# Kernel tuning notes

Hardware: AMD Instinct MI355X
Metric: run time of the kernel (lower is better)

Reference implementation:

```python
import jax, jax.numpy as jnp
import numpy as np

H = 8          # number of heads
D_MODEL = 512  # model dim
D_HEAD = D_MODEL // H


def setup_inputs() -> dict:
    key = jax.random.key(0)
    ks = jax.random.split(key, 8)
    B, C, L = 4, D_MODEL, 2048
    s = 1.0 / np.sqrt(D_MODEL)
    return {
        "x1": jax.random.normal(ks[0], (B, C, L), dtype=jnp.float32),
        "x2": jax.random.normal(ks[1], (B, C, L), dtype=jnp.float32),
        "Wq": jax.random.uniform(ks[2], (D_MODEL, D_MODEL), jnp.float32, -s, s),
        "bq": jax.random.uniform(ks[3], (D_MODEL,), jnp.float32, -s, s),
        "Wk": jax.random.uniform(ks[4], (D_MODEL, D_MODEL), jnp.float32, -s, s),
        "bk": jax.random.uniform(ks[5], (D_MODEL,), jnp.float32, -s, s),
        "Wv": jax.random.uniform(ks[6], (D_MODEL, D_MODEL), jnp.float32, -s, s),
        "bv": jax.random.uniform(ks[7], (D_MODEL,), jnp.float32, -s, s),
    }


def reference(x1, x2, Wq, bq, Wk, bk, Wv, bv):
    # x1, x2: [B, C, L] with C == d_model (3D branch of the torch module)
    B, C, L = x1.shape
    x1t = jnp.swapaxes(x1, 1, 2)  # [B, L, C]
    x2t = jnp.swapaxes(x2, 1, 2)  # [B, L, C]

    def proj(x, W, b):  # torch Linear: x @ W.T + b, then split heads
        y = jnp.einsum('blc,dc->bld', x, W) + b          # [B, L, C]
        return y.reshape(B, -1, H, D_HEAD).transpose(0, 2, 1, 3)  # [B, H, L, d]

    q = proj(x1t, Wq, bq)
    k = proj(x2t, Wk, bk)
    v = proj(x2t, Wv, bv)

    scores = jnp.einsum('bhqd,bhkd->bhqk', q, k) / jnp.sqrt(
        jnp.asarray(D_HEAD, dtype=q.dtype))
    attn = jax.nn.softmax(scores, axis=-1)
    out = jnp.einsum('bhqk,bhkd->bhqd', attn, v)          # [B, H, L, d]

    # transpose(1,2).view(B,-1,C).transpose(1,2) -> [B, C, L]
    out = out.transpose(0, 2, 1, 3).reshape(B, L, C)
    return jnp.swapaxes(out, 1, 2)
```

## Files before the change

kernel.cpp:

```cpp
#include <hip/hip_runtime.h>
#include <hip/hip_bf16.h>

#define L_SEQ 2048
#define DM 512

typedef short bf16x8 __attribute__((ext_vector_type(8)));
typedef float f32x4 __attribute__((ext_vector_type(4)));
typedef float f32x16 __attribute__((ext_vector_type(16)));
typedef unsigned short u16;
typedef u16 u16x8 __attribute__((ext_vector_type(8)));
typedef u16 u16x4 __attribute__((ext_vector_type(4)));
typedef unsigned int u32x2 __attribute__((ext_vector_type(2)));

__device__ __forceinline__ u16 f2bf(float f) {
    unsigned int u = __float_as_uint(f);
    u += 0x7fffu + ((u >> 16) & 1u);
    return (u16)(u >> 16);
}

__device__ __forceinline__ unsigned int pk_bf16(float a, float b) {
    __hip_bfloat162 h = __float22bfloat162_rn(float2{a, b});
    unsigned int u;
    __builtin_memcpy(&u, &h, 4);
    return u;
}

__device__ __forceinline__ void lds_load16(const void* g, void* l) {
    __builtin_amdgcn_global_load_lds(
        (const __attribute__((address_space(1))) unsigned int*)g,
        (__attribute__((address_space(3))) unsigned int*)l,
        16, 0, 0);
}

__device__ __forceinline__ f32x16 zero16() {
    f32x16 z;
#pragma unroll
    for (int i = 0; i < 16; ++i) z[i] = 0.f;
    return z;
}

__global__ void prep(const float* __restrict__ x1, const float* __restrict__ x2,
                     const float* __restrict__ Wq, const float* __restrict__ Wk,
                     const float* __restrict__ Wv,
                     u16* __restrict__ xT, u16* __restrict__ Wall) {
    __shared__ u16 t[128 * 136];
    const int tid = threadIdx.x;
    if (blockIdx.z == 8) {
        int gid = (blockIdx.y * 16 + blockIdx.x) * 256 + tid;
#pragma unroll
        for (int p = 0; p < 12; ++p) {
            int i = p * 16384 + gid;
            int which = i >> 16, j = i & 65535;
            const float* src = (which == 0) ? Wq : (which == 1 ? Wk : Wv);
            float4 v = ((const float4*)src)[j];
            ushort4 o;
            o.x = f2bf(v.x); o.y = f2bf(v.y); o.z = f2bf(v.z); o.w = f2bf(v.w);
            ((ushort4*)Wall)[i] = o;
        }
        return;
    }
    const int z = blockIdx.z, b = z & 3, c0 = blockIdx.y * 128, l0 = blockIdx.x * 128;
    const float* src = (z < 4) ? x1 : x2;
    u16* dbase = xT + (size_t)(z >> 2) * 4194304;
    const float* sp = src + ((size_t)b * DM + c0) * L_SEQ + l0;
#pragma unroll
    for (int p = 0; p < 16; ++p) {
        int id = p * 256 + tid;
        int ci = id >> 5, f4 = id & 31;
        float4 v = *(const float4*)(sp + (size_t)ci * L_SEQ + f4 * 4);
        u16x4 o;
        o[0] = f2bf(v.x); o[1] = f2bf(v.y); o[2] = f2bf(v.z); o[3] = f2bf(v.w);
        *(u16x4*)(t + ci * 136 + f4 * 4) = o;
    }
    __syncthreads();
    u16* dp = dbase + ((size_t)b * L_SEQ + l0) * DM + c0;
#pragma unroll
    for (int p = 0; p < 8; ++p) {
        int id = p * 256 + tid;
        int lj = id >> 4, c8 = id & 15;
        u16x8 o;
#pragma unroll
        for (int i = 0; i < 8; ++i) o[i] = t[(c8 * 8 + i) * 136 + lj];
        *(u16x8*)(dp + (size_t)lj * DM + c8 * 8) = o;
    }
}

#define PROJ_BODY(AB, BB, NAB, NBB, DO_STAGE)                                   \
    {                                                                           \
        __syncthreads();                                                        \
        if (DO_STAGE) {                                                         \
            lds_load16(pA0, smem + (NAB) + sd0);                                \
            lds_load16(pA1, smem + (NAB) + sd1);                                \
            lds_load16(pB0, smem + (NBB) + sd0);                                \
            lds_load16(pB1, smem + (NBB) + sd1);                                \
            pA0 += 32; pA1 += 32; pB0 += 32; pB1 += 32;                         \
        }                                                                       \
        bf16x8 af[4], bfr[4];                                                   \
        _Pragma("unroll")                                                       \
        for (int mt = 0; mt < 4; ++mt)                                          \
            af[mt] = *(const bf16x8*)(smem + (AB) + aoffb[mt]);                 \
        _Pragma("unroll")                                                       \
        for (int nt = 0; nt < 4; ++nt)                                          \
            bfr[nt] = *(const bf16x8*)(smem + (BB) + boffb[nt]);                \
        _Pragma("unroll")                                                       \
        for (int mt = 0; mt < 4; ++mt)                                          \
            _Pragma("unroll")                                                   \
            for (int nt = 0; nt < 4; ++nt)                                      \
                acc[mt][nt] = __builtin_amdgcn_mfma_f32_16x16x32_bf16(          \
                    af[mt], bfr[nt], acc[mt][nt], 0, 0, 0);                     \
    }

__launch_bounds__(256, 3)
__global__ void proj_gemm(const u16* __restrict__ x1T, const u16* __restrict__ x2T,
                          const u16* __restrict__ Wall,
                          const float* __restrict__ bq, const float* __restrict__ bk,
                          const float* __restrict__ bv,
                          u16* __restrict__ Qo, u16* __restrict__ Ko, u16* __restrict__ Vto) {
    __shared__ __align__(16) char smem[34816];
    const int by = blockIdx.y;
    const int b = by / 3, pj = by % 3;
    const int m0 = (blockIdx.x >> 2) * 128, n0 = (blockIdx.x & 3) * 128;
    const u16* xT = (pj == 0) ? x1T : x2T;
    const u16* W = Wall + (size_t)pj * 262144;
    const float* bias = (pj == 0) ? bq : (pj == 1 ? bk : bv);
    const float scale = (pj == 0) ? 0.18033688011112042f : 1.0f;

    const int tid = threadIdx.x;
    const int w = tid >> 6, lane = tid & 63;
    const int lm = lane & 15, lq = lane >> 4;
    const int wrow = (w & 1) * 64, wcol = (w >> 1) * 64;

    const u16 *pA0, *pA1, *pB0, *pB1;
    {
        int s0 = tid, r0 = s0 >> 2, c0 = (s0 & 3) ^ (r0 & 3);
        int s1 = 256 + tid, r1 = s1 >> 2, c1 = (s1 & 3) ^ (r1 & 3);
        pA0 = xT + ((size_t)b * L_SEQ + m0 + r0) * DM + c0 * 8;
        pA1 = xT + ((size_t)b * L_SEQ + m0 + r1) * DM + c1 * 8;
        pB0 = W + (size_t)(n0 + r0) * DM + c0 * 8;
        pB1 = W + (size_t)(n0 + r1) * DM + c1 * 8;
    }
    const int sd0 = w * 1024;
    const int sd1 = 4096 + w * 1024;

    int aoffb[4], boffb[4];
#pragma unroll
    for (int mt = 0; mt < 4; ++mt) {
        int r = wrow + mt * 16 + lm;
        aoffb[mt] = r * 64 + (lq ^ (r & 3)) * 16;
    }
#pragma unroll
    for (int nt = 0; nt < 4; ++nt) {
        int r = wcol + nt * 16 + lm;
        boffb[nt] = r * 64 + (lq ^ (r & 3)) * 16;
    }

    f32x4 acc[4][4];
#pragma unroll
    for (int mt = 0; mt < 4; ++mt)
#pragma unroll
        for (int nt = 0; nt < 4; ++nt) acc[mt][nt] = (f32x4){0.f, 0.f, 0.f, 0.f};

    lds_load16(pA0, smem + 0 + sd0);
    lds_load16(pA1, smem + 0 + sd1);
    lds_load16(pB0, smem + 8192 + sd0);
    lds_load16(pB1, smem + 8192 + sd1);
    pA0 += 32; pA1 += 32; pB0 += 32; pB1 += 32;

    for (int kt2 = 0; kt2 < 8; ++kt2) {
        PROJ_BODY(0, 8192, 16384, 24576, true)
        PROJ_BODY(16384, 24576, 0, 8192, (kt2 < 7))
    }

    float bvv[4];
#pragma unroll
    for (int nt = 0; nt < 4; ++nt) bvv[nt] = bias[n0 + wcol + nt * 16 + lm];

    if (pj < 2) {
        u16* dst = (pj == 0) ? Qo : Ko;
#pragma unroll
        for (int mt = 0; mt < 4; ++mt)
#pragma unroll
            for (int nt = 0; nt < 4; ++nt) {
                int col = n0 + wcol + nt * 16 + lm;
#pragma unroll
                for (int r = 0; r < 4; ++r) {
                    int row = m0 + wrow + mt * 16 + lq * 4 + r;
                    dst[((size_t)b * L_SEQ + row) * DM + col] = f2bf((acc[mt][nt][r] + bvv[nt]) * scale);
                }
            }
    } else {
        __syncthreads();
        u16* epi = (u16*)smem;
#pragma unroll
        for (int mt = 0; mt < 4; ++mt)
#pragma unroll
            for (int nt = 0; nt < 4; ++nt) {
                int colL = wcol + nt * 16 + lm;
                int row0 = wrow + mt * 16 + lq * 4;
                u16x4 tv;
#pragma unroll
                for (int r = 0; r < 4; ++r) tv[r] = f2bf(acc[mt][nt][r] + bvv[nt]);
                *(u16x4*)(epi + colL * 136 + row0) = tv;
            }
        __syncthreads();
#pragma unroll
        for (int p = 0; p < 8; ++p) {
            int id = p * 256 + tid;
            int rr = id >> 4, ch = id & 15;
            u16x8 vv = *(const u16x8*)(epi + rr * 136 + ch * 8);
            *(u16x8*)(Vto + ((size_t)b * DM + n0 + rr) * L_SEQ + m0 + ch * 8) = vv;
        }
    }
}

#define ATTN_BODY(KB, VB, VMC, DO_STAGE)                                        \
    {                                                                           \
        asm volatile("s_waitcnt vmcnt(" #VMC ")" ::: "memory");                 \
        __builtin_amdgcn_s_barrier();                                           \
        bf16x8 af0 = *(const bf16x8*)(smem + (KB) + koffb[0]);                  \
        __builtin_amdgcn_s_setprio(1);                                          \
        f32x16 s = __builtin_amdgcn_mfma_f32_32x32x16_bf16(af0, qf[0], z16,     \
                                                           0, 0, 0);            \
        _Pragma("unroll")                                                       \
        for (int c = 1; c < 4; ++c) {                                           \
            bf16x8 af = *(const bf16x8*)(smem + (KB) + koffb[c]);               \
            s = __builtin_amdgcn_mfma_f32_32x32x16_bf16(af, qf[c], s, 0, 0, 0); \
        }                                                                       \
        __builtin_amdgcn_s_setprio(0);                                          \
        uint2 pw[4];                                                            \
        _Pragma("unroll")                                                       \
        for (int g2 = 0; g2 < 4; ++g2) {                                        \
            float p0 = __builtin_amdgcn_exp2f(s[4 * g2 + 0]);                   \
            float p1 = __builtin_amdgcn_exp2f(s[4 * g2 + 1]);                   \
            float p2 = __builtin_amdgcn_exp2f(s[4 * g2 + 2]);                   \
            float p3 = __builtin_amdgcn_exp2f(s[4 * g2 + 3]);                   \
            l_part += (p0 + p1) + (p2 + p3);                                    \
            pw[g2].x = pk_bf16(p0, p1);                                         \
            pw[g2].y = pk_bf16(p2, p3);                                         \
        }                                                                       \
        __builtin_amdgcn_s_setprio(1);                                          \
        _Pragma("unroll")                                                       \
        for (int c2 = 0; c2 < 2; ++c2) {                                        \
            uint2 pa = pw[2 * c2], pb = pw[2 * c2 + 1];                         \
            u32x2 rx = __builtin_amdgcn_permlane32_swap(pa.x, pb.x, false, false); \
            u32x2 ry = __builtin_amdgcn_permlane32_swap(pa.y, pb.y, false, false); \
            uint4 pu;                                                           \
            pu.x = rx[0]; pu.y = ry[0]; pu.z = rx[1]; pu.w = ry[1];             \
            bf16x8 pf;                                                          \
            __builtin_memcpy(&pf, &pu, 16);                                     \
            _Pragma("unroll")                                                   \
            for (int dt = 0; dt < 2; ++dt) {                                    \
                bf16x8 vf = *(const bf16x8*)(smem + (VB) + voffb[c2 * 2 + dt]); \
                o_acc[dt] = __builtin_amdgcn_mfma_f32_32x32x16_bf16(            \
                    pf, vf, o_acc[dt], 0, 0, 0);                                \
            }                                                                   \
        }                                                                       \
        __builtin_amdgcn_s_setprio(0);                                          \
        asm volatile("s_waitcnt lgkmcnt(0)" ::: "memory");                      \
        __builtin_amdgcn_s_barrier();                                           \
        if (DO_STAGE) {                                                         \
            lds_load16(pKn, smem + (KB) + sdb);                                 \
            lds_load16(pVn, smem + (VB) + sdb);                                 \
            pKn += 64 * DM; pVn += 64;                                          \
        }                                                                       \
    }

__launch_bounds__(512, 4)
__global__ void attn(const u16* __restrict__ Q, const u16* __restrict__ K,
                     const u16* __restrict__ Vt, float* __restrict__ out) {
    __shared__ __align__(16) char smem[50176];
    float* l_lds = (float*)(smem + 49152);
    float* o_lds = (float*)smem;

    const int i = blockIdx.x;
    const int g = i & 7, r_ = i >> 3;
    const int qb = r_ & 15, bh = ((r_ >> 4) << 3) + g;
    const int h_ = bh >> 2, b = bh & 3;

    const int tid = threadIdx.x, w = tid >> 6, lane = tid & 63;
    const int q0 = qb * 128;
    const int lm32 = lane & 31, hi = lane >> 5;
    const int qg = w & 3, hk = w >> 2;
    const int qrow = qg * 32 + lm32;

    const u16* Qb = Q + ((size_t)b * L_SEQ + q0) * DM + h_ * 64;
    const u16* Kb = K + (size_t)b * L_SEQ * DM + h_ * 64;
    const u16* Vb = Vt + ((size_t)b * DM + h_ * 64) * L_SEQ;

    const u16 *pKn, *pVn;
    const int sdb = w * 1024;
    {
        int r = tid >> 3, cc = (tid & 7) ^ (r & 7);
        pKn = Kb + (size_t)r * DM + cc * 8;
        pVn = Vb + (size_t)r * L_SEQ + cc * 8;
    }

    const int rk = hk * 32 + lm32;
    int koffb[4], voffb[4];
#pragma unroll
    for (int c = 0; c < 4; ++c)
        koffb[c] = rk * 128 + ((2 * c + hi) ^ (rk & 7)) * 16;
#pragma unroll
    for (int c2 = 0; c2 < 2; ++c2)
#pragma unroll
        for (int dt = 0; dt < 2; ++dt) {
            int d = dt * 32 + lm32;
            int kc = hk * 4 + c2 * 2 + hi;
            voffb[c2 * 2 + dt] = d * 128 + (kc ^ (d & 7)) * 16;
        }

#pragma unroll
    for (int j = 0; j < 2; ++j) {
        int s = j * 512 + tid;
        int r = s >> 3, cc = (s & 7) ^ (r & 7);
        lds_load16(Qb + (size_t)r * DM + cc * 8, smem + j * 8192 + sdb);
    }
    __syncthreads();
    bf16x8 qf[4];
#pragma unroll
    for (int c = 0; c < 4; ++c) {
        int slot = (2 * c + hi) ^ (qrow & 7);
        qf[c] = *(const bf16x8*)(smem + qrow * 128 + slot * 16);
    }
    __syncthreads();

    float l_part = 0.f;
    const f32x16 z16 = zero16();
    f32x16 o_acc[2];
    o_acc[0] = zero16(); o_acc[1] = zero16();

    lds_load16(pKn, smem + 0 + sdb);     lds_load16(pVn, smem + 24576 + sdb); pKn += 64 * DM; pVn += 64;
    lds_load16(pKn, smem + 8192 + sdb);  lds_load16(pVn, smem + 32768 + sdb); pKn += 64 * DM; pVn += 64;
    lds_load16(pKn, smem + 16384 + sdb); lds_load16(pVn, smem + 40960 + sdb); pKn += 64 * DM; pVn += 64;

    for (int kt3 = 0; kt3 < 10; ++kt3) {
        ATTN_BODY(0,     24576, 4, true)
        ATTN_BODY(8192,  32768, 4, true)
        ATTN_BODY(16384, 40960, 4, (kt3 < 9))
    }
    ATTN_BODY(0,    24576, 2, false)
    ATTN_BODY(8192, 32768, 0, false)

    l_part += __shfl_xor(l_part, 32);

    __syncthreads();
    if (hi == 0) l_lds[hk * 128 + qrow] = l_part;
    if (hk == 0) {
#pragma unroll
        for (int dt = 0; dt < 2; ++dt) {
            int d = dt * 32 + lm32;
#pragma unroll
            for (int g2 = 0; g2 < 4; ++g2) {
                f32x4 vq;
#pragma unroll
                for (int r = 0; r < 4; ++r) vq[r] = o_acc[dt][4 * g2 + r];
                *(f32x4*)(o_lds + d * 132 + qg * 32 + 8 * g2 + 4 * hi) = vq;
            }
        }
    }
    __syncthreads();
    if (hk == 1) {
#pragma unroll
        for (int dt = 0; dt < 2; ++dt) {
            int d = dt * 32 + lm32;
#pragma unroll
            for (int g2 = 0; g2 < 4; ++g2) {
                float* ad = o_lds + d * 132 + qg * 32 + 8 * g2 + 4 * hi;
                f32x4 cur = *(f32x4*)ad;
#pragma unroll
                for (int r = 0; r < 4; ++r) cur[r] += o_acc[dt][4 * g2 + r];
                *(f32x4*)ad = cur;
            }
        }
    }
    __syncthreads();
    float* ob = out + ((size_t)b * DM + h_ * 64) * L_SEQ + q0;
#pragma unroll
    for (int p = 0; p < 4; ++p) {
        int id = p * 512 + tid;
        int d = id >> 5, rc = id & 31;
        f32x4 vv = *(const f32x4*)(o_lds + d * 132 + rc * 4);
        f32x4 la = *(const f32x4*)(l_lds + rc * 4);
        f32x4 lb = *(const f32x4*)(l_lds + 128 + rc * 4);
#pragma unroll
        for (int j = 0; j < 4; ++j) vv[j] *= 1.0f / (la[j] + lb[j]);
        *(f32x4*)(ob + (size_t)d * L_SEQ + rc * 4) = vv;
    }
}

extern "C" void kernel_launch(void* const* d_in, const int* in_sizes, int n_in,
                              void* d_out, int out_size, void* d_ws, size_t ws_size,
                              hipStream_t stream) {
    const float* x1 = (const float*)d_in[0];
    const float* x2 = (const float*)d_in[1];
    const float* Wq = (const float*)d_in[2];
    const float* bq = (const float*)d_in[3];
    const float* Wk = (const float*)d_in[4];
    const float* bk = (const float*)d_in[5];
    const float* Wv = (const float*)d_in[6];
    const float* bv = (const float*)d_in[7];
    float* out = (float*)d_out;

    char* ws = (char*)d_ws;
    u16* x1T = (u16*)(ws);
    u16* x2T = (u16*)(ws + 8388608);
    u16* Wall = (u16*)(ws + 16777216);
    u16* Qb  = (u16*)(ws + 18350080);
    u16* Kb  = (u16*)(ws + 26738688);
    u16* Vtb = (u16*)(ws + 35127296);

    prep<<<dim3(16, 4, 9), 256, 0, stream>>>(x1, x2, Wq, Wk, Wv, x1T, Wall);
    proj_gemm<<<dim3(64, 12), 256, 0, stream>>>(x1T, x2T, Wall, bq, bk, bv, Qb, Kb, Vtb);
    attn<<<512, 512, 0, stream>>>(Qb, Kb, Vtb, out);
}
```

Baseline: 160.6 us.

## Halve attention block to 4 waves, each computing two 32-row Q subtiles

The attention kernel now uses 256 threads (4 waves) per block instead of 8. Each wave processes two 32-row query subtiles that share the same K fragment loads from LDS, and each thread stages twice as many K/V bytes per tile with adjusted vmcnt waits. This raises per-wave MFMA work per LDS read and halves barrier participants. The cost is doubled accumulator and register pressure, and fewer waves available to hide latency.

```diff
diff --git a/kernel.cpp b/kernel.cpp
--- a/kernel.cpp
+++ b/kernel.cpp
@@ -217,55 +217,73 @@
     {                                                                           \
         asm volatile("s_waitcnt vmcnt(" #VMC ")" ::: "memory");                 \
         __builtin_amdgcn_s_barrier();                                           \
-        bf16x8 af0 = *(const bf16x8*)(smem + (KB) + koffb[0]);                  \
-        __builtin_amdgcn_s_setprio(1);                                          \
-        f32x16 s = __builtin_amdgcn_mfma_f32_32x32x16_bf16(af0, qf[0], z16,     \
-                                                           0, 0, 0);            \
+        f32x16 s0, s1;                                                          \
+        {                                                                       \
+            bf16x8 af = *(const bf16x8*)(smem + (KB) + koffb[0]);               \
+            __builtin_amdgcn_s_setprio(1);                                      \
+            s0 = __builtin_amdgcn_mfma_f32_32x32x16_bf16(af, qf[0][0], z16, 0, 0, 0); \
+            s1 = __builtin_amdgcn_mfma_f32_32x32x16_bf16(af, qf[1][0], z16, 0, 0, 0); \
+        }                                                                       \
         _Pragma("unroll")                                                       \
         for (int c = 1; c < 4; ++c) {                                           \
             bf16x8 af = *(const bf16x8*)(smem + (KB) + koffb[c]);               \
-            s = __builtin_amdgcn_mfma_f32_32x32x16_bf16(af, qf[c], s, 0, 0, 0); \
+            s0 = __builtin_amdgcn_mfma_f32_32x32x16_bf16(af, qf[0][c], s0, 0, 0, 0); \
+            s1 = __builtin_amdgcn_mfma_f32_32x32x16_bf16(af, qf[1][c], s1, 0, 0, 0); \
         }                                                                       \
         __builtin_amdgcn_s_setprio(0);                                          \
-        uint2 pw[4];                                                            \
+        uint2 pw0[4], pw1[4];                                                   \
         _Pragma("unroll")                                                       \
         for (int g2 = 0; g2 < 4; ++g2) {                                        \
-            float p0 = __builtin_amdgcn_exp2f(s[4 * g2 + 0]);                   \
-            float p1 = __builtin_amdgcn_exp2f(s[4 * g2 + 1]);                   \
-            float p2 = __builtin_amdgcn_exp2f(s[4 * g2 + 2]);                   \
-            float p3 = __builtin_amdgcn_exp2f(s[4 * g2 + 3]);                   \
-            l_part += (p0 + p1) + (p2 + p3);                                    \
-            pw[g2].x = pk_bf16(p0, p1);                                         \
-            pw[g2].y = pk_bf16(p2, p3);                                         \
+            float a0 = __builtin_amdgcn_exp2f(s0[4 * g2 + 0]);                  \
+            float a1 = __builtin_amdgcn_exp2f(s0[4 * g2 + 1]);                  \
+            float a2 = __builtin_amdgcn_exp2f(s0[4 * g2 + 2]);                  \
+            float a3 = __builtin_amdgcn_exp2f(s0[4 * g2 + 3]);                  \
+            l_part0 += (a0 + a1) + (a2 + a3);                                   \
+            pw0[g2].x = pk_bf16(a0, a1);                                        \
+            pw0[g2].y = pk_bf16(a2, a3);                                        \
+            float b0 = __builtin_amdgcn_exp2f(s1[4 * g2 + 0]);                  \
+            float b1 = __builtin_amdgcn_exp2f(s1[4 * g2 + 1]);                  \
+            float b2 = __builtin_amdgcn_exp2f(s1[4 * g2 + 2]);                  \
+            float b3 = __builtin_amdgcn_exp2f(s1[4 * g2 + 3]);                  \
+            l_part1 += (b0 + b1) + (b2 + b3);                                   \
+            pw1[g2].x = pk_bf16(b0, b1);                                        \
+            pw1[g2].y = pk_bf16(b2, b3);                                        \
         }                                                                       \
         __builtin_amdgcn_s_setprio(1);                                          \
         _Pragma("unroll")                                                       \
         for (int c2 = 0; c2 < 2; ++c2) {                                        \
-            uint2 pa = pw[2 * c2], pb = pw[2 * c2 + 1];                         \
-            u32x2 rx = __builtin_amdgcn_permlane32_swap(pa.x, pb.x, false, false); \
-            u32x2 ry = __builtin_amdgcn_permlane32_swap(pa.y, pb.y, false, false); \
-            uint4 pu;                                                           \
-            pu.x = rx[0]; pu.y = ry[0]; pu.z = rx[1]; pu.w = ry[1];             \
-            bf16x8 pf;                                                          \
-            __builtin_memcpy(&pf, &pu, 16);                                     \
+            u32x2 r0x = __builtin_amdgcn_permlane32_swap(pw0[2 * c2].x, pw0[2 * c2 + 1].x, false, false); \
+            u32x2 r0y = __builtin_amdgcn_permlane32_swap(pw0[2 * c2].y, pw0[2 * c2 + 1].y, false, false); \
+            u32x2 r1x = __builtin_amdgcn_permlane32_swap(pw1[2 * c2].x, pw1[2 * c2 + 1].x, false, false); \
+            u32x2 r1y = __builtin_amdgcn_permlane32_swap(pw1[2 * c2].y, pw1[2 * c2 + 1].y, false, false); \
+            uint4 pu0, pu1;                                                     \
+            pu0.x = r0x[0]; pu0.y = r0y[0]; pu0.z = r0x[1]; pu0.w = r0y[1];     \
+            pu1.x = r1x[0]; pu1.y = r1y[0]; pu1.z = r1x[1]; pu1.w = r1y[1];     \
+            bf16x8 pf0, pf1;                                                    \
+            __builtin_memcpy(&pf0, &pu0, 16);                                   \
+            __builtin_memcpy(&pf1, &pu1, 16);                                   \
             _Pragma("unroll")                                                   \
             for (int dt = 0; dt < 2; ++dt) {                                    \
                 bf16x8 vf = *(const bf16x8*)(smem + (VB) + voffb[c2 * 2 + dt]); \
-                o_acc[dt] = __builtin_amdgcn_mfma_f32_32x32x16_bf16(            \
-                    pf, vf, o_acc[dt], 0, 0, 0);                                \
+                o_acc[0][dt] = __builtin_amdgcn_mfma_f32_32x32x16_bf16(         \
+                    pf0, vf, o_acc[0][dt], 0, 0, 0);                            \
+                o_acc[1][dt] = __builtin_amdgcn_mfma_f32_32x32x16_bf16(         \
+                    pf1, vf, o_acc[1][dt], 0, 0, 0);                            \
             }                                                                   \
         }                                                                       \
         __builtin_amdgcn_s_setprio(0);                                          \
         asm volatile("s_waitcnt lgkmcnt(0)" ::: "memory");                      \
         __builtin_amdgcn_s_barrier();                                           \
         if (DO_STAGE) {                                                         \
-            lds_load16(pKn, smem + (KB) + sdb);                                 \
-            lds_load16(pVn, smem + (VB) + sdb);                                 \
-            pKn += 64 * DM; pVn += 64;                                          \
-        }                                                                       \
-    }
-
-__launch_bounds__(512, 4)
+            lds_load16(pK0, smem + (KB) + sdb);                                 \
+            lds_load16(pK1, smem + (KB) + 4096 + sdb);                          \
+            lds_load16(pV0, smem + (VB) + sdb);                                 \
+            lds_load16(pV1, smem + (VB) + 4096 + sdb);                          \
+            pK0 += 64 * DM; pK1 += 64 * DM; pV0 += 64; pV1 += 64;               \
+        }                                                                       \
+    }
+
+__launch_bounds__(256, 2)
 __global__ void attn(const u16* __restrict__ Q, const u16* __restrict__ K,
                      const u16* __restrict__ Vt, float* __restrict__ out) {
     __shared__ __align__(16) char smem[50176];
@@ -280,19 +298,20 @@
     const int tid = threadIdx.x, w = tid >> 6, lane = tid & 63;
     const int q0 = qb * 128;
     const int lm32 = lane & 31, hi = lane >> 5;
-    const int qg = w & 3, hk = w >> 2;
-    const int qrow = qg * 32 + lm32;
+    const int qg = w & 1, hk = w >> 1;
 
     const u16* Qb = Q + ((size_t)b * L_SEQ + q0) * DM + h_ * 64;
     const u16* Kb = K + (size_t)b * L_SEQ * DM + h_ * 64;
     const u16* Vb = Vt + ((size_t)b * DM + h_ * 64) * L_SEQ;
 
-    const u16 *pKn, *pVn;
+    const u16 *pK0, *pK1, *pV0, *pV1;
     const int sdb = w * 1024;
     {
         int r = tid >> 3, cc = (tid & 7) ^ (r & 7);
-        pKn = Kb + (size_t)r * DM + cc * 8;
-        pVn = Vb + (size_t)r * L_SEQ + cc * 8;
+        pK0 = Kb + (size_t)r * DM + cc * 8;
+        pK1 = Kb + (size_t)(32 + r) * DM + cc * 8;
+        pV0 = Vb + (size_t)r * L_SEQ + cc * 8;
+        pV1 = Vb + (size_t)(32 + r) * L_SEQ + cc * 8;
     }
 
     const int rk = hk * 32 + lm32;
@@ -310,74 +329,92 @@
         }
 
 #pragma unroll
-    for (int j = 0; j < 2; ++j) {
-        int s = j * 512 + tid;
+    for (int j = 0; j < 4; ++j) {
+        int s = j * 256 + tid;
         int r = s >> 3, cc = (s & 7) ^ (r & 7);
-        lds_load16(Qb + (size_t)r * DM + cc * 8, smem + j * 8192 + sdb);
-    }
-    __syncthreads();
-    bf16x8 qf[4];
-#pragma unroll
-    for (int c = 0; c < 4; ++c) {
-        int slot = (2 * c + hi) ^ (qrow & 7);
-        qf[c] = *(const bf16x8*)(smem + qrow * 128 + slot * 16);
-    }
-    __syncthreads();
-
-    float l_part = 0.f;
+        lds_load16(Qb + (size_t)r * DM + cc * 8, smem + j * 4096 + sdb);
+    }
+    __syncthreads();
+    bf16x8 qf[2][4];
+#pragma unroll
+    for (int sub = 0; sub < 2; ++sub) {
+        int qrow_s = qg * 64 + sub * 32 + lm32;
+#pragma unroll
+        for (int c = 0; c < 4; ++c) {
+            int slot = (2 * c + hi) ^ (qrow_s & 7);
+            qf[sub][c] = *(const bf16x8*)(smem + qrow_s * 128 + slot * 16);
+        }
+    }
+    __syncthreads();
+
+    float l_part0 = 0.f, l_part1 = 0.f;
     const f32x16 z16 = zero16();
-    f32x16 o_acc[2];
-    o_acc[0] = zero16(); o_acc[1] = zero16();
-
-    lds_load16(pKn, smem + 0 + sdb);     lds_load16(pVn, smem + 24576 + sdb); pKn += 64 * DM; pVn += 64;
-    lds_load16(pKn, smem + 8192 + sdb);  lds_load16(pVn, smem + 32768 + sdb); pKn += 64 * DM; pVn += 64;
-    lds_load16(pKn, smem + 16384 + sdb); lds_load16(pVn, smem + 40960 + sdb); pKn += 64 * DM; pVn += 64;
+    f32x16 o_acc[2][2];
+    o_acc[0][0] = zero16(); o_acc[0][1] = zero16();
+    o_acc[1][0] = zero16(); o_acc[1][1] = zero16();
+
+#pragma unroll
+    for (int t = 0; t < 3; ++t) {
+        lds_load16(pK0, smem + t * 8192 + sdb);
+        lds_load16(pK1, smem + t * 8192 + 4096 + sdb);
+        lds_load16(pV0, smem + 24576 + t * 8192 + sdb);
+        lds_load16(pV1, smem + 24576 + t * 8192 + 4096 + sdb);
+        pK0 += 64 * DM; pK1 += 64 * DM; pV0 += 64; pV1 += 64;
+    }
 
     for (int kt3 = 0; kt3 < 10; ++kt3) {
-        ATTN_BODY(0,     24576, 4, true)
-        ATTN_BODY(8192,  32768, 4, true)
-        ATTN_BODY(16384, 40960, 4, (kt3 < 9))
-    }
-    ATTN_BODY(0,    24576, 2, false)
+        ATTN_BODY(0,     24576, 8, true)
+        ATTN_BODY(8192,  32768, 8, true)
+        ATTN_BODY(16384, 40960, 8, (kt3 < 9))
+    }
+    ATTN_BODY(0,    24576, 4, false)
     ATTN_BODY(8192, 32768, 0, false)
 
-    l_part += __shfl_xor(l_part, 32);
-
-    __syncthreads();
-    if (hi == 0) l_lds[hk * 128 + qrow] = l_part;
+    l_part0 += __shfl_xor(l_part0, 32);
+    l_part1 += __shfl_xor(l_part1, 32);
+
+    __syncthreads();
+    if (hi == 0) {
+        l_lds[hk * 128 + qg * 64 + lm32] = l_part0;
+        l_lds[hk * 128 + qg * 64 + 32 + lm32] = l_part1;
+    }
     if (hk == 0) {
 #pragma unroll
-        for (int dt = 0; dt < 2; ++dt) {
-            int d = dt * 32 + lm32;
-#pragma unroll
-            for (int g2 = 0; g2 < 4; ++g2) {
-                f32x4 vq;
-#pragma unroll
-                for (int r = 0; r < 4; ++r) vq[r] = o_acc[dt][4 * g2 + r];
-                *(f32x4*)(o_lds + d * 132 + qg * 32 + 8 * g2 + 4 * hi) = vq;
+        for (int sub = 0; sub < 2; ++sub)
+#pragma unroll
+            for (int dt = 0; dt < 2; ++dt) {
+                int d = dt * 32 + lm32;
+#pragma unroll
+                for (int g2 = 0; g2 < 4; ++g2) {
+                    f32x4 vq;
+#pragma unroll
+                    for (int r = 0; r < 4; ++r) vq[r] = o_acc[sub][dt][4 * g2 + r];
+                    *(f32x4*)(o_lds + d * 132 + qg * 64 + sub * 32 + 8 * g2 + 4 * hi) = vq;
+                }
             }
-        }
     }
     __syncthreads();
     if (hk == 1) {
 #pragma unroll
-        for (int dt = 0; dt < 2; ++dt) {
-            int d = dt * 32 + lm32;
-#pragma unroll
-            for (int g2 = 0; g2 < 4; ++g2) {
-                float* ad = o_lds + d * 132 + qg * 32 + 8 * g2 + 4 * hi;
-                f32x4 cur = *(f32x4*)ad;
-#pragma unroll
-                for (int r = 0; r < 4; ++r) cur[r] += o_acc[dt][4 * g2 + r];
-                *(f32x4*)ad = cur;
+        for (int sub = 0; sub < 2; ++sub)
+#pragma unroll
+            for (int dt = 0; dt < 2; ++dt) {
+                int d = dt * 32 + lm32;
+#pragma unroll
+                for (int g2 = 0; g2 < 4; ++g2) {
+                    float* ad = o_lds + d * 132 + qg * 64 + sub * 32 + 8 * g2 + 4 * hi;
+                    f32x4 cur = *(f32x4*)ad;
+#pragma unroll
+                    for (int r = 0; r < 4; ++r) cur[r] += o_acc[sub][dt][4 * g2 + r];
+                    *(f32x4*)ad = cur;
+                }
             }
-        }
     }
     __syncthreads();
     float* ob = out + ((size_t)b * DM + h_ * 64) * L_SEQ + q0;
 #pragma unroll
-    for (int p = 0; p < 4; ++p) {
-        int id = p * 512 + tid;
+    for (int p = 0; p < 8; ++p) {
+        int id = p * 256 + tid;
         int d = id >> 5, rc = id & 31;
         f32x4 vv = *(const f32x4*)(o_lds + d * 132 + rc * 4);
         f32x4 la = *(const f32x4*)(l_lds + rc * 4);
@@ -411,5 +448,5 @@
 
     prep<<<dim3(16, 4, 9), 256, 0, stream>>>(x1, x2, Wq, Wk, Wv, x1T, Wall);
     proj_gemm<<<dim3(64, 12), 256, 0, stream>>>(x1T, x2T, Wall, bq, bk, bv, Qb, Kb, Vtb);
-    attn<<<512, 512, 0, stream>>>(Qb, Kb, Vtb, out);
-}
+    attn<<<512, 256, 0, stream>>>(Qb, Kb, Vtb, out);
+}
```

Result: no change. 158.0 us (-1.6%).

## Software-pipeline QK^T of next tile with softmax and PV of current tile

Applied to the files above, without the earlier changes.

Restructures the attention inner loop so the QK^T MFMAs for the next K tile are issued in the same step as the exp2/bf16 packing and PV MFMAs of the current tile, using two ping-ponged score registers. The K staging buffer is decoupled from the consumption buffer, and the vmcnt waits and prologue/epilogue are adjusted. The aim is to hide the transcendental and permlane latency behind matrix work. In exchange it raises register pressure with an extra 16-float accumulator, which could hurt occupancy at 4 blocks of 512 threads, and it makes the buffer indexing more fragile.

```diff
diff --git a/kernel.cpp b/kernel.cpp
--- a/kernel.cpp
+++ b/kernel.cpp
@@ -213,27 +213,29 @@
     }
 }
 
-#define ATTN_BODY(KB, VB, VMC, DO_STAGE)                                        \
+#define ATTN_QK(KNB, SDST)                                                      \
     {                                                                           \
-        asm volatile("s_waitcnt vmcnt(" #VMC ")" ::: "memory");                 \
-        __builtin_amdgcn_s_barrier();                                           \
-        bf16x8 af0 = *(const bf16x8*)(smem + (KB) + koffb[0]);                  \
+        bf16x8 af0 = *(const bf16x8*)(smem + (KNB) + koffb[0]);                 \
+        bf16x8 af1 = *(const bf16x8*)(smem + (KNB) + koffb[1]);                 \
+        bf16x8 af2 = *(const bf16x8*)(smem + (KNB) + koffb[2]);                 \
+        bf16x8 af3 = *(const bf16x8*)(smem + (KNB) + koffb[3]);                 \
         __builtin_amdgcn_s_setprio(1);                                          \
-        f32x16 s = __builtin_amdgcn_mfma_f32_32x32x16_bf16(af0, qf[0], z16,     \
-                                                           0, 0, 0);            \
-        _Pragma("unroll")                                                       \
-        for (int c = 1; c < 4; ++c) {                                           \
-            bf16x8 af = *(const bf16x8*)(smem + (KB) + koffb[c]);               \
-            s = __builtin_amdgcn_mfma_f32_32x32x16_bf16(af, qf[c], s, 0, 0, 0); \
-        }                                                                       \
+        SDST = __builtin_amdgcn_mfma_f32_32x32x16_bf16(af0, qf[0], z16, 0, 0, 0); \
+        SDST = __builtin_amdgcn_mfma_f32_32x32x16_bf16(af1, qf[1], SDST, 0, 0, 0); \
+        SDST = __builtin_amdgcn_mfma_f32_32x32x16_bf16(af2, qf[2], SDST, 0, 0, 0); \
+        SDST = __builtin_amdgcn_mfma_f32_32x32x16_bf16(af3, qf[3], SDST, 0, 0, 0); \
         __builtin_amdgcn_s_setprio(0);                                          \
+    }
+
+#define ATTN_SMPV(VB, SCUR)                                                     \
+    {                                                                           \
         uint2 pw[4];                                                            \
         _Pragma("unroll")                                                       \
         for (int g2 = 0; g2 < 4; ++g2) {                                        \
-            float p0 = __builtin_amdgcn_exp2f(s[4 * g2 + 0]);                   \
-            float p1 = __builtin_amdgcn_exp2f(s[4 * g2 + 1]);                   \
-            float p2 = __builtin_amdgcn_exp2f(s[4 * g2 + 2]);                   \
-            float p3 = __builtin_amdgcn_exp2f(s[4 * g2 + 3]);                   \
+            float p0 = __builtin_amdgcn_exp2f(SCUR[4 * g2 + 0]);                \
+            float p1 = __builtin_amdgcn_exp2f(SCUR[4 * g2 + 1]);                \
+            float p2 = __builtin_amdgcn_exp2f(SCUR[4 * g2 + 2]);                \
+            float p3 = __builtin_amdgcn_exp2f(SCUR[4 * g2 + 3]);                \
             l_part += (p0 + p1) + (p2 + p3);                                    \
             pw[g2].x = pk_bf16(p0, p1);                                         \
             pw[g2].y = pk_bf16(p2, p3);                                         \
@@ -241,9 +243,8 @@
         __builtin_amdgcn_s_setprio(1);                                          \
         _Pragma("unroll")                                                       \
         for (int c2 = 0; c2 < 2; ++c2) {                                        \
-            uint2 pa = pw[2 * c2], pb = pw[2 * c2 + 1];                         \
-            u32x2 rx = __builtin_amdgcn_permlane32_swap(pa.x, pb.x, false, false); \
-            u32x2 ry = __builtin_amdgcn_permlane32_swap(pa.y, pb.y, false, false); \
+            u32x2 rx = __builtin_amdgcn_permlane32_swap(pw[2 * c2].x, pw[2 * c2 + 1].x, false, false); \
+            u32x2 ry = __builtin_amdgcn_permlane32_swap(pw[2 * c2].y, pw[2 * c2 + 1].y, false, false); \
             uint4 pu;                                                           \
             pu.x = rx[0]; pu.y = ry[0]; pu.z = rx[1]; pu.w = ry[1];             \
             bf16x8 pf;                                                          \
@@ -256,10 +257,18 @@
             }                                                                   \
         }                                                                       \
         __builtin_amdgcn_s_setprio(0);                                          \
+    }
+
+#define ATTN_BODY(KNB, VB, VMC, DO_STAGE, KSB, SCUR, SNXT)                      \
+    {                                                                           \
+        asm volatile("s_waitcnt vmcnt(" #VMC ")" ::: "memory");                 \
+        __builtin_amdgcn_s_barrier();                                           \
+        ATTN_QK(KNB, SNXT)                                                      \
+        ATTN_SMPV(VB, SCUR)                                                     \
         asm volatile("s_waitcnt lgkmcnt(0)" ::: "memory");                      \
         __builtin_amdgcn_s_barrier();                                           \
         if (DO_STAGE) {                                                         \
-            lds_load16(pKn, smem + (KB) + sdb);                                 \
+            lds_load16(pKn, smem + (KSB) + sdb);                                \
             lds_load16(pVn, smem + (VB) + sdb);                                 \
             pKn += 64 * DM; pVn += 64;                                          \
         }                                                                       \
@@ -333,13 +342,21 @@
     lds_load16(pKn, smem + 8192 + sdb);  lds_load16(pVn, smem + 32768 + sdb); pKn += 64 * DM; pVn += 64;
     lds_load16(pKn, smem + 16384 + sdb); lds_load16(pVn, smem + 40960 + sdb); pKn += 64 * DM; pVn += 64;
 
-    for (int kt3 = 0; kt3 < 10; ++kt3) {
-        ATTN_BODY(0,     24576, 4, true)
-        ATTN_BODY(8192,  32768, 4, true)
-        ATTN_BODY(16384, 40960, 4, (kt3 < 9))
-    }
-    ATTN_BODY(0,    24576, 2, false)
-    ATTN_BODY(8192, 32768, 0, false)
+    f32x16 sA, sB;
+    asm volatile("s_waitcnt vmcnt(4)" ::: "memory");
+    __builtin_amdgcn_s_barrier();
+    ATTN_QK(0, sA)
+
+    for (int kt6 = 0; kt6 < 5; ++kt6) {
+        ATTN_BODY(8192,  24576, 2, true, 0,            sA, sB)
+        ATTN_BODY(16384, 32768, 2, true, 8192,         sB, sA)
+        ATTN_BODY(0,     40960, 2, true, 16384,        sA, sB)
+        ATTN_BODY(8192,  24576, 2, true, 0,            sB, sA)
+        ATTN_BODY(16384, 32768, 2, true, 8192,         sA, sB)
+        ATTN_BODY(0,     40960, 2, (kt6 < 4), 16384,   sB, sA)
+    }
+    ATTN_BODY(8192, 24576, 0, false, 0, sA, sB)
+    ATTN_SMPV(32768, sB)
 
     l_part += __shfl_xor(l_part, 32);
 
```

After: 172.1 us. 7.1% more time.
